# Kernel tuning notes

Hardware: AMD Instinct MI355X
Metric: run time of the kernel (lower is better)

## Reference

```python
import jax, jax.numpy as jnp
import numpy as np

B, N, D, H, IN, HID = 16, 1024, 256, 8, 256, 1024
HD = IN // H  # head dim = 32
EPS = 1e-5


def layer_norm(x, g, b):
    mu = jnp.mean(x, axis=-1, keepdims=True)
    var = jnp.var(x, axis=-1, keepdims=True)
    return (x - mu) / jnp.sqrt(var + EPS) * g + b


def setup_inputs() -> dict:
    key = jax.random.key(0)
    ks = jax.random.split(key, 12)
    s = 0.02
    return {
        "x": jax.random.normal(ks[0], (B, N, D), jnp.float32),
        "coords": jax.random.normal(ks[1], (B, N, 2), jnp.float32),
        "g1": jnp.ones((D,), jnp.float32),
        "b1": jnp.zeros((D,), jnp.float32),
        "Wqkv": jax.random.normal(ks[2], (3 * IN, D), jnp.float32) * s,
        "Wproj": jax.random.normal(ks[3], (IN, IN), jnp.float32) * s,
        "bproj": jnp.zeros((IN,), jnp.float32),
        "g2": jnp.ones((D,), jnp.float32),
        "b2": jnp.zeros((D,), jnp.float32),
        "W1": jax.random.normal(ks[4], (HID, D), jnp.float32) * s,
        "bb1": jnp.zeros((HID,), jnp.float32),
        "W2": jax.random.normal(ks[5], (D, HID), jnp.float32) * s,
        "bb2": jnp.zeros((D,), jnp.float32),
    }


def reference(x, coords, g1, b1, Wqkv, Wproj, bproj, g2, b2, W1, bb1, W2, bb2):
    # ---- Attention branch (pre-norm) ----
    h = layer_norm(x, g1, b1)                       # [B,N,D]
    qkv = h @ Wqkv.T                                # [B,N,3*IN]
    qkv = qkv.reshape(B, N, 3, H, HD).transpose(2, 0, 3, 1, 4)  # [3,B,H,N,HD]
    q, k, v = qkv[0], qkv[1], qkv[2]
    scale = HD ** -0.5
    attn = jnp.einsum('bhid,bhjd->bhij', q * scale, k)  # [B,H,N,N]
    attn = jax.nn.softmax(attn, axis=-1)
    o = jnp.einsum('bhij,bhjd->bhid', attn, v)      # [B,H,N,HD]
    o = o.transpose(0, 2, 1, 3).reshape(B, N, IN)   # [B,N,IN]
    o = o @ Wproj.T + bproj
    o = o + h                                       # residual inside Attention (vs normed input)
    x = x + o                                       # Block residual (double residual, faithful)
    # ---- MLP branch ----
    h2 = layer_norm(x, g2, b2)
    m = jax.nn.gelu(h2 @ W1.T + bb1, approximate=False) @ W2.T + bb2
    return x + m
```

## Files before the change

kernel.cpp:

```cpp
#include <hip/hip_runtime.h>
#include <hip/hip_bf16.h>
#include <math.h>

#define Bdim 16
#define Ndim 1024
#define Ddim 256
#define Hdim 8
#define HDdim 32
#define INdim 256
#define HIDdim 1024
#define Tdim (Bdim * Ndim)

typedef __attribute__((ext_vector_type(8)))  short bf16x8;
typedef __attribute__((ext_vector_type(4)))  short bf16x4;
typedef __attribute__((ext_vector_type(16))) float f32x16;
typedef unsigned int u32;

__device__ inline short f2bf(float x) {
    union { __hip_bfloat16 b; short s; } u;
    u.b = __float2bfloat16(x);
    return u.s;
}

__device__ inline float bf2f(short s) {
    return __uint_as_float(((u32)(unsigned short)s) << 16);
}

__device__ inline float fexp2(float x) {
#if __has_builtin(__builtin_amdgcn_exp2f)
    return __builtin_amdgcn_exp2f(x);
#else
    return exp2f(x);
#endif
}

__device__ inline u32 pack2bf(float a, float b) {
#if __has_builtin(__builtin_amdgcn_cvt_pk_bf16_f32)
    typedef __attribute__((ext_vector_type(2))) __bf16 bf16x2_t;
    union { bf16x2_t v; u32 u; } c;
    c.v = __builtin_amdgcn_cvt_pk_bf16_f32(a, b);
    return c.u;
#else
    u32 ua = __float_as_uint(a), ub = __float_as_uint(b);
    return ((ua + 0x8000u) >> 16) | ((ub + 0x8000u) & 0xffff0000u);
#endif
}

__device__ inline void plswap(u32 &a, u32 &b) {
    asm volatile("v_permlane32_swap_b32 %0, %1" : "+v"(a), "+v"(b));
}

__device__ inline float gelu_exact(float v) {
    return 0.5f * v * (1.0f + erff(v * 0.70710678118654752f));
}

__device__ inline void bar_nodrain() {
    asm volatile("s_waitcnt lgkmcnt(0)" ::: "memory");
    __builtin_amdgcn_s_barrier();
    asm volatile("" ::: "memory");
}

#define N4_QKV  (3 * INdim * Ddim / 4)
#define N4_PROJ (INdim * INdim / 4)
#define N4_W1   (HIDdim * Ddim / 4)
#define N4_W2   (Ddim * HIDdim / 4)

__global__ __launch_bounds__(256) void cvt_all_kernel(const float* __restrict__ s0,
                                                      const float* __restrict__ s1,
                                                      const float* __restrict__ s2,
                                                      const float* __restrict__ s3,
                                                      short* __restrict__ d0,
                                                      short* __restrict__ d1,
                                                      short* __restrict__ d2,
                                                      short* __restrict__ d3) {
    int i = blockIdx.x * 256 + threadIdx.x;
    const float* src; short* dst; int j;
    if (i < N4_QKV)                          { src = s0; dst = d0; j = i; }
    else if (i < N4_QKV + N4_PROJ)           { src = s1; dst = d1; j = i - N4_QKV; }
    else if (i < N4_QKV + N4_PROJ + N4_W1)   { src = s2; dst = d2; j = i - N4_QKV - N4_PROJ; }
    else                                     { src = s3; dst = d3; j = i - N4_QKV - N4_PROJ - N4_W1; }
    float4 v = ((const float4*)src)[j];
    bf16x4 b;
    b[0] = f2bf(v.x); b[1] = f2bf(v.y); b[2] = f2bf(v.z); b[3] = f2bf(v.w);
    ((bf16x4*)dst)[j] = b;
}

__global__ __launch_bounds__(256) void ln4_kernel(const float* __restrict__ x,
                                                  const float* __restrict__ g,
                                                  const float* __restrict__ b,
                                                  float* __restrict__ outf,
                                                  short* __restrict__ outb) {
    int w = threadIdx.x >> 6, lane = threadIdx.x & 63;
    int row = blockIdx.x * 4 + w;
    float4 v = ((const float4*)x)[(size_t)row * 64 + lane];
    float s  = (v.x + v.y) + (v.z + v.w);
    float s2 = (v.x * v.x + v.y * v.y) + (v.z * v.z + v.w * v.w);
    #pragma unroll
    for (int off = 32; off; off >>= 1) {
        s  += __shfl_xor(s,  off, 64);
        s2 += __shfl_xor(s2, off, 64);
    }
    float mu   = s * (1.0f / Ddim);
    float var  = s2 * (1.0f / Ddim) - mu * mu;
    float rstd = rsqrtf(var + 1e-5f);
    float4 gg = ((const float4*)g)[lane];
    float4 bb = ((const float4*)b)[lane];
    float4 r;
    r.x = (v.x - mu) * rstd * gg.x + bb.x;
    r.y = (v.y - mu) * rstd * gg.y + bb.y;
    r.z = (v.z - mu) * rstd * gg.z + bb.z;
    r.w = (v.w - mu) * rstd * gg.w + bb.w;
    if (outf) ((float4*)outf)[(size_t)row * 64 + lane] = r;
    bf16x4 rb;
    rb[0] = f2bf(r.x); rb[1] = f2bf(r.y); rb[2] = f2bf(r.z); rb[3] = f2bf(r.w);
    ((bf16x4*)outb)[(size_t)row * 64 + lane] = rb;
}

#define EPI_NONE 0
#define EPI_PROJ 1
#define EPI_GELU 2
#define EPI_RES  3
#define EPI_QKV  4

#define GPAD32 40
#define SCALE2Q 0.25505654249892417f

__device__ inline bf16x8 comb8(bf16x8 a, bf16x8 b, float rl) {
    bf16x8 r;
    #pragma unroll
    for (int i = 0; i < 8; ++i) r[i] = f2bf((bf2f(a[i]) + bf2f(b[i])) * rl);
    return r;
}

template <int EPI, int BN, bool COMB>
__global__ __launch_bounds__(256) void gemm_mfma(const short* __restrict__ A,
                                                 const short* __restrict__ W,
                                                 void* __restrict__ Cv,
                                                 int M, int N, int K,
                                                 const float* __restrict__ bias,
                                                 const float* __restrict__ add1,
                                                 const float* __restrict__ add2,
                                                 const float* __restrict__ lpc) {
    __shared__ short As[2][64 * GPAD32];
    __shared__ short Bs[2][BN * GPAD32];
    const int tid = threadIdx.x, w = tid >> 6, lane = tid & 63;
    const int col = lane & 31;
    const int half_id = lane >> 5;

    const int nbx = gridDim.x;
    const int flat = blockIdx.y * nbx + blockIdx.x;
    const int cpx = (nbx * (int)gridDim.y) >> 3;
    const int swz = (flat & 7) * cpx + (flat >> 3);
    const int m0 = (swz / nbx) * 64, n0 = (swz % nbx) * BN;

    const int wm = (w & 1) * 32;
    const int wn = (BN == 128) ? (w >> 1) * 64 : (w >> 1) * 32;
    constexpr int TN = (BN == 128) ? 2 : 1;

    f32x16 acc[TN];
    #pragma unroll
    for (int t = 0; t < TN; ++t) acc[t] = 0.0f;

    const int sra = tid >> 2, ssa = (tid & 3) * 8;
    const int srb = (BN == 128) ? (tid >> 1) : (tid >> 2);
    const int ssb = (BN == 128) ? (tid & 1) * 16 : (tid & 3) * 8;
    constexpr int NB = (BN == 128) ? 2 : 1;

    const short* pAsrc = &A[(size_t)(m0 + sra) * K + ssa];
    const short* pBsrc = &W[(size_t)(n0 + srb) * K + ssb];
    const float* lpr0 = COMB ? (lpc + (size_t)(m0 + sra) * 8) : nullptr;
    const float* lpr1 = COMB ? (lpr0 + (size_t)Tdim * 8) : nullptr;

    bf16x8 ax, ax2, bx[NB];  float lx = 0.0f;
    bf16x8 ay, ay2, by[NB];  float ly = 0.0f;

    auto LOADSET = [&](bf16x8& aa, bf16x8& aa2, float& ll, bf16x8* bb, int t) {
        const short* ap = pAsrc + t * 32;
        aa = *(const bf16x8*)ap;
        if constexpr (COMB) {
            aa2 = *(const bf16x8*)(ap + (size_t)Tdim * 256);
            ll = lpr0[t] + lpr1[t];
        }
        #pragma unroll
        for (int j = 0; j < NB; ++j) bb[j] = *(const bf16x8*)&pBsrc[t * 32 + j * 8];
    };
    auto WRITESET = [&](int buf, bf16x8 aa, bf16x8 aa2, float ll, const bf16x8* bb) {
        bf16x8 av = aa;
        if constexpr (COMB) av = comb8(aa, aa2, 1.0f / ll);
        *(bf16x8*)&As[buf][sra * GPAD32 + ssa] = av;
        #pragma unroll
        for (int j = 0; j < NB; ++j) *(bf16x8*)&Bs[buf][srb * GPAD32 + ssb + j * 8] = bb[j];
    };
    auto COMPUTEB = [&](int buf) {
        #pragma unroll
        for (int ks = 0; ks < 2; ++ks) {
            bf16x8 af = *(const bf16x8*)&As[buf][(wm + col) * GPAD32 + ks * 16 + half_id * 8];
            bf16x8 bfv[TN];
            #pragma unroll
            for (int t = 0; t < TN; ++t)
                bfv[t] = *(const bf16x8*)&Bs[buf][(wn + t * 32 + col) * GPAD32 + ks * 16 + half_id * 8];
            #pragma unroll
            for (int t = 0; t < TN; ++t)
                acc[t] = __builtin_amdgcn_mfma_f32_32x32x16_bf16(af, bfv[t], acc[t], 0, 0, 0);
        }
    };

    const int T = K >> 5;

    LOADSET(ax, ax2, lx, bx, 0);
    LOADSET(ay, ay2, ly, by, 1);
    WRITESET(0, ax, ax2, lx, bx);
    LOADSET(ax, ax2, lx, bx, 2);
    bar_nodrain();

    for (int kt2 = 0; kt2 < T; kt2 += 2) {
        WRITESET(1, ay, ay2, ly, by);
        if (kt2 + 3 < T) LOADSET(ay, ay2, ly, by, kt2 + 3);
        COMPUTEB(0);
        bar_nodrain();
        if (kt2 + 2 < T) WRITESET(0, ax, ax2, lx, bx);
        if (kt2 + 4 < T) LOADSET(ax, ax2, lx, bx, kt2 + 4);
        COMPUTEB(1);
        bar_nodrain();
    }

    float* Cf = (float*)Cv;
    short* Cb = (short*)Cv;
    #pragma unroll
    for (int r = 0; r < 16; ++r) {
        int row = m0 + wm + (r & 3) + 8 * (r >> 2) + 4 * half_id;
        #pragma unroll
        for (int t = 0; t < TN; ++t) {
            int cn = n0 + wn + t * 32 + col;
            size_t off = (size_t)row * N + cn;
            float v = acc[t][r];
            if (EPI != EPI_NONE && EPI != EPI_QKV) v += bias[cn];
            if (EPI == EPI_QKV && cn < 256) v *= SCALE2Q;
            if (EPI == EPI_GELU) v = gelu_exact(v);
            if (EPI == EPI_PROJ) v += add1[off] + add2[off];
            if (EPI == EPI_RES)  v += add1[off];
            if (EPI == EPI_PROJ || EPI == EPI_RES) Cf[off] = v;
            else                                   Cb[off] = f2bf(v);
        }
    }
}

#define VTPAD 136

__global__ __launch_bounds__(256) void vtrans_kernel(const short* __restrict__ qkv,
                                                     short* __restrict__ vT) {
    __shared__ short Tl[32 * VTPAD];
    const int tid = threadIdx.x;
    const int bh = blockIdx.x, c = blockIdx.y;
    const int b = bh >> 3, head = bh & 7;
    {
        int r = tid >> 1, hv = tid & 1;
        const short* src = qkv + (size_t)b * Ndim * 768 + (size_t)(c * 128 + r) * 768
                           + 512 + head * 32 + hv * 16;
        bf16x8 v0 = *(const bf16x8*)&src[0];
        bf16x8 v1 = *(const bf16x8*)&src[8];
        #pragma unroll
        for (int i = 0; i < 8; ++i) {
            Tl[(hv * 16 + i) * VTPAD + r]     = v0[i];
            Tl[(hv * 16 + 8 + i) * VTPAD + r] = v1[i];
        }
    }
    __syncthreads();
    {
        int d = tid >> 3, j16 = (tid & 7) * 16;
        short* dst = vT + (size_t)(bh * 32 + d) * Ndim + c * 128 + j16;
        *(bf16x8*)&dst[0] = *(const bf16x8*)&Tl[d * VTPAD + j16];
        *(bf16x8*)&dst[8] = *(const bf16x8*)&Tl[d * VTPAD + j16 + 8];
    }
}

#define KVPAD 40
#define CHUNK 128

__global__ __launch_bounds__(256) void attn_mfma_kernel(const short* __restrict__ qkv,
                                                        const short* __restrict__ vT,
                                                        short* __restrict__ opart,
                                                        float* __restrict__ lpart) {
    __shared__ short Ks[CHUNK * KVPAD];
    __shared__ short Vt[32 * VTPAD];

    const int tid = threadIdx.x;
    const int w = tid >> 6;
    const int lane = tid & 63;
    const int col = lane & 31;
    const int half_id = lane >> 5;

    const int bh = blockIdx.y;
    const int b = bh >> 3, head = bh & 7;
    const int q0w = blockIdx.x * 128 + w * 32;
    const int part = blockIdx.z;

    const size_t qkvb = (size_t)b * Ndim * 768;
    short* op = opart + (size_t)part * Tdim * 256;
    float* lp = lpart + (size_t)part * Tdim * 8;

    const int sr = tid >> 1, shv = tid & 1;
    const short* ksrc = qkv + qkvb + (size_t)sr * 768 + 256 + head * 32 + shv * 16;
    const int sd = tid >> 3, sj16 = (tid & 7) * 16;
    const short* vsrc = vT + (size_t)(bh * 32 + sd) * Ndim + sj16;

    bf16x8 qf[2];
    {
        const short* qrow = qkv + qkvb + (size_t)(q0w + col) * 768 + head * 32;
        #pragma unroll
        for (int kh = 0; kh < 2; ++kh)
            qf[kh] = *(const bf16x8*)&qrow[kh * 16 + half_id * 8];
    }

    bf16x8 vone;
    #pragma unroll
    for (int i = 0; i < 8; ++i) vone[i] = (short)0x3F80;

    f32x16 o_acc = 0.0f, l_acc = 0.0f;

    const int c0 = part * 4;

    bf16x8 rk0, rk1, rv0, rv1;
    {
        const short* kp = ksrc + (size_t)(c0 * CHUNK) * 768;
        rk0 = *(const bf16x8*)&kp[0];
        rk1 = *(const bf16x8*)&kp[8];
        const short* vp = vsrc + c0 * CHUNK;
        rv0 = *(const bf16x8*)&vp[0];
        rv1 = *(const bf16x8*)&vp[8];
    }

    #pragma unroll
    for (int ci = 0; ci < 4; ++ci) {
        if (ci != 0) __syncthreads();
        *(bf16x8*)&Ks[sr * KVPAD + shv * 16]     = rk0;
        *(bf16x8*)&Ks[sr * KVPAD + shv * 16 + 8] = rk1;
        *(bf16x8*)&Vt[sd * VTPAD + sj16]     = rv0;
        *(bf16x8*)&Vt[sd * VTPAD + sj16 + 8] = rv1;
        __syncthreads();

        if (ci < 3) {
            const short* kp = ksrc + (size_t)((c0 + ci + 1) * CHUNK) * 768;
            rk0 = *(const bf16x8*)&kp[0];
            rk1 = *(const bf16x8*)&kp[8];
            const short* vp = vsrc + (c0 + ci + 1) * CHUNK;
            rv0 = *(const bf16x8*)&vp[0];
            rv1 = *(const bf16x8*)&vp[8];
        }

        f32x16 s_cur;
        {
            bf16x8 kf0 = *(bf16x8*)&Ks[col * KVPAD + half_id * 8];
            bf16x8 kf1 = *(bf16x8*)&Ks[col * KVPAD + 16 + half_id * 8];
            f32x16 z = 0.0f;
            z = __builtin_amdgcn_mfma_f32_32x32x16_bf16(kf0, qf[0], z, 0, 0, 0);
            z = __builtin_amdgcn_mfma_f32_32x32x16_bf16(kf1, qf[1], z, 0, 0, 0);
            s_cur = z;
        }
        #pragma unroll
        for (int jt = 0; jt < 4; ++jt) {
            f32x16 s_next;
            if (jt < 3) {
                bf16x8 kf0 = *(bf16x8*)&Ks[((jt + 1) * 32 + col) * KVPAD + half_id * 8];
                bf16x8 kf1 = *(bf16x8*)&Ks[((jt + 1) * 32 + col) * KVPAD + 16 + half_id * 8];
                f32x16 z = 0.0f;
                z = __builtin_amdgcn_mfma_f32_32x32x16_bf16(kf0, qf[0], z, 0, 0, 0);
                z = __builtin_amdgcn_mfma_f32_32x32x16_bf16(kf1, qf[1], z, 0, 0, 0);
                s_next = z;
            }

            bf16x8 vf0 = *(bf16x8*)&Vt[col * VTPAD + jt * 32 + half_id * 8];
            bf16x8 vf1 = *(bf16x8*)&Vt[col * VTPAD + jt * 32 + 16 + half_id * 8];

            u32 wd[8];
            #pragma unroll
            for (int g = 0; g < 8; ++g) {
                float e0 = fexp2(s_cur[2 * g + 0]);
                float e1 = fexp2(s_cur[2 * g + 1]);
                wd[g] = pack2bf(e0, e1);
            }
            plswap(wd[0], wd[2]); plswap(wd[1], wd[3]);
            plswap(wd[4], wd[6]); plswap(wd[5], wd[7]);

            union { u32 u[4]; bf16x8 v; } p0, p1;
            p0.u[0] = wd[0]; p0.u[1] = wd[1]; p0.u[2] = wd[2]; p0.u[3] = wd[3];
            p1.u[0] = wd[4]; p1.u[1] = wd[5]; p1.u[2] = wd[6]; p1.u[3] = wd[7];

            __builtin_amdgcn_s_setprio(1);
            o_acc = __builtin_amdgcn_mfma_f32_32x32x16_bf16(p0.v, vf0, o_acc, 0, 0, 0);
            o_acc = __builtin_amdgcn_mfma_f32_32x32x16_bf16(p1.v, vf1, o_acc, 0, 0, 0);
            l_acc = __builtin_amdgcn_mfma_f32_32x32x16_bf16(p0.v, vone, l_acc, 0, 0, 0);
            l_acc = __builtin_amdgcn_mfma_f32_32x32x16_bf16(p1.v, vone, l_acc, 0, 0, 0);
            __builtin_amdgcn_s_setprio(0);

            if (jt < 3) s_cur = s_next;
        }
    }

    #pragma unroll
    for (int r = 0; r < 16; ++r) {
        int q_r = (r & 3) + 8 * (r >> 2) + 4 * half_id;
        size_t gq = (size_t)(b * Ndim + q0w + q_r);
        op[gq * INdim + head * 32 + col] = f2bf(o_acc[r]);
    }
    if (col < 16) {
        int r = col;
        int q_r = (r & 3) + 8 * (r >> 2) + 4 * half_id;
        lp[(size_t)(b * Ndim + q0w + q_r) * 8 + head] = l_acc[r];
    }
}

extern "C" void kernel_launch(void* const* d_in, const int* in_sizes, int n_in,
                              void* d_out, int out_size, void* d_ws, size_t ws_size,
                              hipStream_t stream) {
    const float* x     = (const float*)d_in[0];
    const float* g1    = (const float*)d_in[2];
    const float* b1    = (const float*)d_in[3];
    const float* Wqkv  = (const float*)d_in[4];
    const float* Wproj = (const float*)d_in[5];
    const float* bproj = (const float*)d_in[6];
    const float* g2    = (const float*)d_in[7];
    const float* b2    = (const float*)d_in[8];
    const float* W1    = (const float*)d_in[9];
    const float* bb1   = (const float*)d_in[10];
    const float* W2    = (const float*)d_in[11];
    const float* bb2   = (const float*)d_in[12];
    float* out = (float*)d_out;

    char* ws = (char*)d_ws;
    float* h      = (float*)(ws);
    short* h_bf   = (short*)(ws + (size_t)(16u << 20));
    short* qkv_bf = (short*)(ws + (size_t)(24u << 20));
    float* xnew   = (float*)(ws + (size_t)(24u << 20));
    short* opart  = (short*)(ws + (size_t)(48u << 20));
    short* mid_bf = (short*)(ws + (size_t)(48u << 20));
    float* lpart  = (float*)(ws + (size_t)(80u << 20));
    short* vT     = (short*)(ws + (size_t)(81u << 20));
    short* wqkv_b = (short*)(ws + (size_t)(89u << 20));
    short* wproj_b= (short*)(ws + (size_t)(89u << 20) + 768 * 1024);
    short* w1_b   = (short*)(ws + (size_t)(90u << 20));
    short* w2_b   = (short*)(ws + (size_t)(90u << 20) + 512 * 1024);

    cvt_all_kernel<<<(N4_QKV + N4_PROJ + N4_W1 + N4_W2 + 255) / 256, 256, 0, stream>>>(
        Wqkv, Wproj, W1, W2, wqkv_b, wproj_b, w1_b, w2_b);

    ln4_kernel<<<Tdim / 4, 256, 0, stream>>>(x, g1, b1, h, h_bf);
    gemm_mfma<EPI_QKV, 128, false><<<dim3(768 / 128, Tdim / 64), 256, 0, stream>>>(
        h_bf, wqkv_b, qkv_bf, Tdim, 768, 256, nullptr, nullptr, nullptr, nullptr);
    vtrans_kernel<<<dim3(Bdim * Hdim, Ndim / 128), 256, 0, stream>>>(qkv_bf, vT);
    attn_mfma_kernel<<<dim3(Ndim / 128, Bdim * Hdim, 2), 256, 0, stream>>>(
        qkv_bf, vT, opart, lpart);
    gemm_mfma<EPI_PROJ, 64, true><<<dim3(256 / 64, Tdim / 64), 256, 0, stream>>>(
        opart, wproj_b, xnew, Tdim, 256, 256, bproj, h, x, lpart);
    ln4_kernel<<<Tdim / 4, 256, 0, stream>>>(xnew, g2, b2, nullptr, h_bf);
    gemm_mfma<EPI_GELU, 128, false><<<dim3(1024 / 128, Tdim / 64), 256, 0, stream>>>(
        h_bf, w1_b, mid_bf, Tdim, 1024, 256, bb1, nullptr, nullptr, nullptr);
    gemm_mfma<EPI_RES, 64, false><<<dim3(256 / 64, Tdim / 64), 256, 0, stream>>>(
        mid_bf, w2_b, out, Tdim, 256, 1024, bb2, xnew, nullptr, nullptr);
}
```

Measured before the change: 216.9 us.

## Fuse LayerNorm2, MLP up-projection with GELU, and down-projection into one kernel

```diff
diff --git a/kernel.cpp b/kernel.cpp
--- a/kernel.cpp
+++ b/kernel.cpp
@@ -245,6 +245,148 @@
     }
 }
 
+#define MPAD  264
+#define W2PAD 72
+
+__global__ __launch_bounds__(256) void mlp_fused_kernel(const float* __restrict__ xnew,
+                                                        const float* __restrict__ g2,
+                                                        const float* __restrict__ b2,
+                                                        const short* __restrict__ W1b,
+                                                        const float* __restrict__ bb1,
+                                                        const short* __restrict__ W2b,
+                                                        const float* __restrict__ bb2,
+                                                        float* __restrict__ out) {
+    __shared__ short h2[64 * MPAD];
+    __shared__ short W1s[64 * MPAD];
+    __shared__ short W2s[256 * W2PAD];
+    __shared__ short Ps[64 * W2PAD];
+
+    const int tid = threadIdx.x, w = tid >> 6, lane = tid & 63;
+    const int col = lane & 31, half_id = lane >> 5;
+    const int m0 = blockIdx.x * 64;
+
+    {
+        float4 gg = ((const float4*)g2)[lane];
+        float4 bb = ((const float4*)b2)[lane];
+        #pragma unroll 4
+        for (int rr = 0; rr < 16; ++rr) {
+            int row = w * 16 + rr;
+            float4 v = ((const float4*)xnew)[(size_t)(m0 + row) * 64 + lane];
+            float s  = (v.x + v.y) + (v.z + v.w);
+            float s2 = (v.x * v.x + v.y * v.y) + (v.z * v.z + v.w * v.w);
+            #pragma unroll
+            for (int off = 32; off; off >>= 1) {
+                s  += __shfl_xor(s,  off, 64);
+                s2 += __shfl_xor(s2, off, 64);
+            }
+            float mu   = s * (1.0f / 256.0f);
+            float var  = s2 * (1.0f / 256.0f) - mu * mu;
+            float rstd = rsqrtf(var + 1e-5f);
+            bf16x4 rb;
+            rb[0] = f2bf((v.x - mu) * rstd * gg.x + bb.x);
+            rb[1] = f2bf((v.y - mu) * rstd * gg.y + bb.y);
+            rb[2] = f2bf((v.z - mu) * rstd * gg.z + bb.z);
+            rb[3] = f2bf((v.w - mu) * rstd * gg.w + bb.w);
+            *(bf16x4*)&h2[row * MPAD + lane * 4] = rb;
+        }
+    }
+
+    const int r1 = tid >> 2, kb1 = (tid & 3) * 64;
+    const short* w1src = W1b + r1 * 256 + kb1;
+    const short* w2src = W2b + (size_t)tid * 1024;
+
+    bf16x8 w1pf0, w1pf1, w1pf2, w1pf3, w1pf4, w1pf5, w1pf6, w1pf7;
+    bf16x8 w2pf0, w2pf1, w2pf2, w2pf3, w2pf4, w2pf5, w2pf6, w2pf7;
+    {
+        const short* p1 = w1src;
+        w1pf0 = *(const bf16x8*)&p1[0];  w1pf1 = *(const bf16x8*)&p1[8];
+        w1pf2 = *(const bf16x8*)&p1[16]; w1pf3 = *(const bf16x8*)&p1[24];
+        w1pf4 = *(const bf16x8*)&p1[32]; w1pf5 = *(const bf16x8*)&p1[40];
+        w1pf6 = *(const bf16x8*)&p1[48]; w1pf7 = *(const bf16x8*)&p1[56];
+        const short* p2 = w2src;
+        w2pf0 = *(const bf16x8*)&p2[0];  w2pf1 = *(const bf16x8*)&p2[8];
+        w2pf2 = *(const bf16x8*)&p2[16]; w2pf3 = *(const bf16x8*)&p2[24];
+        w2pf4 = *(const bf16x8*)&p2[32]; w2pf5 = *(const bf16x8*)&p2[40];
+        w2pf6 = *(const bf16x8*)&p2[48]; w2pf7 = *(const bf16x8*)&p2[56];
+    }
+
+    f32x16 acc_out[4];
+    #pragma unroll
+    for (int t = 0; t < 4; ++t) acc_out[t] = 0.0f;
+
+    const int rows1 = 32 * (w >> 1), cols1 = 32 * (w & 1);
+    const int rows2 = 32 * (w & 1),  cols2 = 128 * (w >> 1);
+
+    bar_nodrain();
+
+    for (int s = 0; s < 16; ++s) {
+        {
+            short* d1 = &W1s[r1 * MPAD + kb1];
+            *(bf16x8*)&d1[0]  = w1pf0; *(bf16x8*)&d1[8]  = w1pf1;
+            *(bf16x8*)&d1[16] = w1pf2; *(bf16x8*)&d1[24] = w1pf3;
+            *(bf16x8*)&d1[32] = w1pf4; *(bf16x8*)&d1[40] = w1pf5;
+            *(bf16x8*)&d1[48] = w1pf6; *(bf16x8*)&d1[56] = w1pf7;
+            short* d2 = &W2s[tid * W2PAD];
+            *(bf16x8*)&d2[0]  = w2pf0; *(bf16x8*)&d2[8]  = w2pf1;
+            *(bf16x8*)&d2[16] = w2pf2; *(bf16x8*)&d2[24] = w2pf3;
+            *(bf16x8*)&d2[32] = w2pf4; *(bf16x8*)&d2[40] = w2pf5;
+            *(bf16x8*)&d2[48] = w2pf6; *(bf16x8*)&d2[56] = w2pf7;
+        }
+        bar_nodrain();
+
+        if (s < 15) {
+            const short* p1 = w1src + (s + 1) * (64 * 256);
+            w1pf0 = *(const bf16x8*)&p1[0];  w1pf1 = *(const bf16x8*)&p1[8];
+            w1pf2 = *(const bf16x8*)&p1[16]; w1pf3 = *(const bf16x8*)&p1[24];
+            w1pf4 = *(const bf16x8*)&p1[32]; w1pf5 = *(const bf16x8*)&p1[40];
+            w1pf6 = *(const bf16x8*)&p1[48]; w1pf7 = *(const bf16x8*)&p1[56];
+            const short* p2 = w2src + (s + 1) * 64;
+            w2pf0 = *(const bf16x8*)&p2[0];  w2pf1 = *(const bf16x8*)&p2[8];
+            w2pf2 = *(const bf16x8*)&p2[16]; w2pf3 = *(const bf16x8*)&p2[24];
+            w2pf4 = *(const bf16x8*)&p2[32]; w2pf5 = *(const bf16x8*)&p2[40];
+            w2pf6 = *(const bf16x8*)&p2[48]; w2pf7 = *(const bf16x8*)&p2[56];
+        }
+
+        f32x16 acc1 = 0.0f;
+        #pragma unroll
+        for (int ks = 0; ks < 16; ++ks) {
+            bf16x8 af  = *(const bf16x8*)&h2[(rows1 + col) * MPAD + ks * 16 + half_id * 8];
+            bf16x8 bfv = *(const bf16x8*)&W1s[(cols1 + col) * MPAD + ks * 16 + half_id * 8];
+            acc1 = __builtin_amdgcn_mfma_f32_32x32x16_bf16(af, bfv, acc1, 0, 0, 0);
+        }
+
+        float bias1 = bb1[s * 64 + cols1 + col];
+        #pragma unroll
+        for (int r = 0; r < 16; ++r) {
+            int pr = rows1 + (r & 3) + 8 * (r >> 2) + 4 * half_id;
+            Ps[pr * W2PAD + cols1 + col] = f2bf(gelu_exact(acc1[r] + bias1));
+        }
+        bar_nodrain();
+
+        #pragma unroll
+        for (int kk = 0; kk < 4; ++kk) {
+            bf16x8 paf = *(const bf16x8*)&Ps[(rows2 + col) * W2PAD + kk * 16 + half_id * 8];
+            #pragma unroll
+            for (int ct = 0; ct < 4; ++ct) {
+                bf16x8 bf2 = *(const bf16x8*)&W2s[(cols2 + 32 * ct + col) * W2PAD + kk * 16 + half_id * 8];
+                acc_out[ct] = __builtin_amdgcn_mfma_f32_32x32x16_bf16(paf, bf2, acc_out[ct], 0, 0, 0);
+            }
+        }
+        bar_nodrain();
+    }
+
+    #pragma unroll
+    for (int r = 0; r < 16; ++r) {
+        int row = m0 + rows2 + (r & 3) + 8 * (r >> 2) + 4 * half_id;
+        #pragma unroll
+        for (int ct = 0; ct < 4; ++ct) {
+            int cn = cols2 + 32 * ct + col;
+            size_t off = (size_t)row * 256 + cn;
+            out[off] = xnew[off] + acc_out[ct][r] + bb2[cn];
+        }
+    }
+}
+
 #define VTPAD 136
 
 __global__ __launch_bounds__(256) void vtrans_kernel(const short* __restrict__ qkv,
@@ -433,7 +575,6 @@
     short* qkv_bf = (short*)(ws + (size_t)(24u << 20));
     float* xnew   = (float*)(ws + (size_t)(24u << 20));
     short* opart  = (short*)(ws + (size_t)(48u << 20));
-    short* mid_bf = (short*)(ws + (size_t)(48u << 20));
     float* lpart  = (float*)(ws + (size_t)(80u << 20));
     short* vT     = (short*)(ws + (size_t)(81u << 20));
     short* wqkv_b = (short*)(ws + (size_t)(89u << 20));
@@ -452,9 +593,6 @@
         qkv_bf, vT, opart, lpart);
     gemm_mfma<EPI_PROJ, 64, true><<<dim3(256 / 64, Tdim / 64), 256, 0, stream>>>(
         opart, wproj_b, xnew, Tdim, 256, 256, bproj, h, x, lpart);
-    ln4_kernel<<<Tdim / 4, 256, 0, stream>>>(xnew, g2, b2, nullptr, h_bf);
-    gemm_mfma<EPI_GELU, 128, false><<<dim3(1024 / 128, Tdim / 64), 256, 0, stream>>>(
-        h_bf, w1_b, mid_bf, Tdim, 1024, 256, bb1, nullptr, nullptr, nullptr);
-    gemm_mfma<EPI_RES, 64, false><<<dim3(256 / 64, Tdim / 64), 256, 0, stream>>>(
-        mid_bf, w2_b, out, Tdim, 256, 1024, bb2, xnew, nullptr, nullptr);
-}
+    mlp_fused_kernel<<<Tdim / 64, 256, 0, stream>>>(
+        xnew, g2, b2, w1_b, bb1, w2_b, bb2, out);
+}
```

Measured after the change: 239.7 us. +10.5%, slower.

## Fuse LayerNorm2, FC1+GELU and FC2+residual into one MLP kernel

Applied to the files above, without the earlier changes.

```diff
diff --git a/kernel.cpp b/kernel.cpp
--- a/kernel.cpp
+++ b/kernel.cpp
@@ -245,6 +245,103 @@
     }
 }
 
+#define MLPAD 264
+#define PSPAD 136
+
+__global__ __launch_bounds__(256) void mlp_fused_kernel(const float* __restrict__ xnew,
+                                                        const float* __restrict__ g2,
+                                                        const float* __restrict__ b2,
+                                                        const short* __restrict__ W1b,
+                                                        const float* __restrict__ bb1,
+                                                        const short* __restrict__ W2b,
+                                                        const float* __restrict__ bb2,
+                                                        float* __restrict__ out) {
+    __shared__ short h2[32 * MLPAD];
+    __shared__ short Ps[32 * PSPAD];
+
+    const int tid = threadIdx.x, w = tid >> 6, lane = tid & 63;
+    const int col = lane & 31, half_id = lane >> 5;
+    const int m0 = blockIdx.x * 32;
+
+    {
+        float4 gg = ((const float4*)g2)[lane];
+        float4 bb = ((const float4*)b2)[lane];
+        #pragma unroll
+        for (int rr = 0; rr < 8; ++rr) {
+            int row = w * 8 + rr;
+            float4 v = ((const float4*)xnew)[(size_t)(m0 + row) * 64 + lane];
+            float s  = (v.x + v.y) + (v.z + v.w);
+            float s2 = (v.x * v.x + v.y * v.y) + (v.z * v.z + v.w * v.w);
+            #pragma unroll
+            for (int off = 32; off; off >>= 1) {
+                s  += __shfl_xor(s,  off, 64);
+                s2 += __shfl_xor(s2, off, 64);
+            }
+            float mu   = s * (1.0f / 256.0f);
+            float var  = s2 * (1.0f / 256.0f) - mu * mu;
+            float rstd = rsqrtf(var + 1e-5f);
+            bf16x4 rb;
+            rb[0] = f2bf((v.x - mu) * rstd * gg.x + bb.x);
+            rb[1] = f2bf((v.y - mu) * rstd * gg.y + bb.y);
+            rb[2] = f2bf((v.z - mu) * rstd * gg.z + bb.z);
+            rb[3] = f2bf((v.w - mu) * rstd * gg.w + bb.w);
+            *(bf16x4*)&h2[row * MLPAD + lane * 4] = rb;
+        }
+    }
+
+    f32x16 acc_out0 = 0.0f, acc_out1 = 0.0f;
+
+    const short* w1p = W1b + (size_t)(w * 32 + col) * 256 + half_id * 8;
+    const short* w2p0 = W2b + (size_t)(w * 64 + col) * 1024 + half_id * 8;
+    const short* w2p1 = W2b + (size_t)(w * 64 + 32 + col) * 1024 + half_id * 8;
+
+    bar_nodrain();
+
+    for (int s = 0; s < 8; ++s) {
+        f32x16 acc1 = 0.0f;
+        const short* w1s = w1p + (size_t)s * 128 * 256;
+        #pragma unroll
+        for (int ks = 0; ks < 16; ++ks) {
+            bf16x8 af  = *(const bf16x8*)&h2[col * MLPAD + ks * 16 + half_id * 8];
+            bf16x8 bfv = *(const bf16x8*)&w1s[ks * 16];
+            acc1 = __builtin_amdgcn_mfma_f32_32x32x16_bf16(af, bfv, acc1, 0, 0, 0);
+        }
+
+        float bias1 = bb1[s * 128 + w * 32 + col];
+        #pragma unroll
+        for (int r = 0; r < 16; ++r) {
+            int pr = (r & 3) + 8 * (r >> 2) + 4 * half_id;
+            Ps[pr * PSPAD + w * 32 + col] = f2bf(gelu_exact(acc1[r] + bias1));
+        }
+        bar_nodrain();
+
+        #pragma unroll
+        for (int kk = 0; kk < 8; ++kk) {
+            bf16x8 paf = *(const bf16x8*)&Ps[col * PSPAD + kk * 16 + half_id * 8];
+            bf16x8 b0 = *(const bf16x8*)&w2p0[s * 128 + kk * 16];
+            bf16x8 b1 = *(const bf16x8*)&w2p1[s * 128 + kk * 16];
+            acc_out0 = __builtin_amdgcn_mfma_f32_32x32x16_bf16(paf, b0, acc_out0, 0, 0, 0);
+            acc_out1 = __builtin_amdgcn_mfma_f32_32x32x16_bf16(paf, b1, acc_out1, 0, 0, 0);
+        }
+        bar_nodrain();
+    }
+
+    #pragma unroll
+    for (int r = 0; r < 16; ++r) {
+        int row = m0 + (r & 3) + 8 * (r >> 2) + 4 * half_id;
+        {
+            int cn = w * 64 + col;
+            size_t off = (size_t)row * 256 + cn;
+            out[off] = xnew[off] + acc_out0[r] + bb2[cn];
+        }
+        {
+            int cn = w * 64 + 32 + col;
+            size_t off = (size_t)row * 256 + cn;
+            out[off] = xnew[off] + acc_out1[r] + bb2[cn];
+        }
+    }
+}
+
 #define VTPAD 136
 
 __global__ __launch_bounds__(256) void vtrans_kernel(const short* __restrict__ qkv,
@@ -433,7 +530,6 @@
     short* qkv_bf = (short*)(ws + (size_t)(24u << 20));
     float* xnew   = (float*)(ws + (size_t)(24u << 20));
     short* opart  = (short*)(ws + (size_t)(48u << 20));
-    short* mid_bf = (short*)(ws + (size_t)(48u << 20));
     float* lpart  = (float*)(ws + (size_t)(80u << 20));
     short* vT     = (short*)(ws + (size_t)(81u << 20));
     short* wqkv_b = (short*)(ws + (size_t)(89u << 20));
@@ -452,9 +548,6 @@
         qkv_bf, vT, opart, lpart);
     gemm_mfma<EPI_PROJ, 64, true><<<dim3(256 / 64, Tdim / 64), 256, 0, stream>>>(
         opart, wproj_b, xnew, Tdim, 256, 256, bproj, h, x, lpart);
-    ln4_kernel<<<Tdim / 4, 256, 0, stream>>>(xnew, g2, b2, nullptr, h_bf);
-    gemm_mfma<EPI_GELU, 128, false><<<dim3(1024 / 128, Tdim / 64), 256, 0, stream>>>(
-        h_bf, w1_b, mid_bf, Tdim, 1024, 256, bb1, nullptr, nullptr, nullptr);
-    gemm_mfma<EPI_RES, 64, false><<<dim3(256 / 64, Tdim / 64), 256, 0, stream>>>(
-        mid_bf, w2_b, out, Tdim, 256, 1024, bb2, xnew, nullptr, nullptr);
-}
+    mlp_fused_kernel<<<Tdim / 32, 256, 0, stream>>>(
+        xnew, g2, b2, w1_b, bb1, w2_b, bb2, out);
+}
```

Result: slower. 243.6 us (+12.3%).
